# Kernel tuning notes

Measured on AMD Instinct MI355X. Metric: run time of the kernel, lower is better.

## Reference

```python
import jax, jax.numpy as jnp
import numpy as np

KNN_K = 16
EPS = 1e-5


def _knn_idx(p, k):
    # p: [B,3,N] -> idx [B,N,k] of nearest neighbors (self excluded)
    pt = jnp.swapaxes(p, 1, 2)                      # [B,N,3]
    xx = jnp.sum(pt * pt, axis=-1)                  # [B,N]
    inner = jnp.einsum('bnd,bmd->bnm', pt, pt)      # [B,N,N]
    dist = -(xx[:, :, None] - 2.0 * inner + xx[:, None, :])  # -||pi-pj||^2
    N = pt.shape[1]
    dist = dist - 1e9 * jnp.eye(N, dtype=dist.dtype)
    return jax.lax.top_k(dist, k)[1]


def _ln(x, g, b):
    mu = jnp.mean(x, axis=-1, keepdims=True)
    var = jnp.mean((x - mu) ** 2, axis=-1, keepdims=True)
    return (x - mu) * jax.lax.rsqrt(var + EPS) * g + b


_gather = jax.vmap(lambda a, i: a[i])  # a:[N,C], i:[N,k] -> [N,k,C]


def setup_inputs() -> dict:
    key = jax.random.key(0)
    ks = jax.random.split(key, 24)
    Cin, C, B, N = 64, 128, 8, 2048
    s = lambda k_, shp, fan: jax.random.normal(k_, shp, jnp.float32) * (1.0 / np.sqrt(fan))
    return {
        'x': jax.random.normal(ks[0], (B, Cin, N), jnp.float32),
        'p': jax.random.normal(ks[1], (B, 3, N), jnp.float32),
        'Win': s(ks[2], (C, Cin), Cin), 'bin_': jnp.zeros((C,), jnp.float32),
        'Wq': s(ks[3], (C, C), C), 'Wk': s(ks[4], (C, C), C), 'Wv': s(ks[5], (C, C), C),
        'Wd1': s(ks[6], (C, 3), 3), 'bd1': jnp.zeros((C,), jnp.float32),
        'Wd2': s(ks[7], (C, C), C), 'bd2': jnp.zeros((C,), jnp.float32),
        'Wa': s(ks[8], (C, C), C), 'ba': jnp.zeros((C,), jnp.float32),
        'g1': jnp.ones((C,), jnp.float32), 'b1': jnp.zeros((C,), jnp.float32),
        'g2': jnp.ones((C,), jnp.float32), 'b2': jnp.zeros((C,), jnp.float32),
        'Wf1': s(ks[9], (4 * C, C), C), 'bf1': jnp.zeros((4 * C,), jnp.float32),
        'Wf2': s(ks[10], (C, 4 * C), 4 * C), 'bf2': jnp.zeros((C,), jnp.float32),
    }


def reference(x, p, Win, bin_, Wq, Wk, Wv, Wd1, bd1, Wd2, bd2, Wa, ba,
              g1, b1, g2, b2, Wf1, bf1, Wf2, bf2) -> jnp.ndarray:
    B, _, N = x.shape
    k = min(KNN_K, max(1, N - 1))
    # in_proj (conv1x1 == per-point linear); work in [B,N,C]
    h = jnp.einsum('oc,bcn->bno', Win, x) + bin_          # [B,N,C]
    hn = _ln(h, g1, b1)
    idx = _knn_idx(p, k)                                  # [B,N,k] (int)
    q = hn @ Wq.T                                         # [B,N,C]
    k_all = hn @ Wk.T
    v_all = hn @ Wv.T
    k_j = _gather(k_all, idx)                             # [B,N,k,C]
    v_j = _gather(v_all, idx)
    pt = jnp.swapaxes(p, 1, 2)                            # [B,N,3]
    p_j = _gather(pt, idx)                                # [B,N,k,3]
    rel = pt[:, :, None, :] - p_j                         # [B,N,k,3]
    d = jax.nn.relu(rel @ Wd1.T + bd1) @ Wd2.T + bd2      # [B,N,k,C]
    logits = (q[:, :, None, :] - k_j + d) @ Wa.T + ba     # [B,N,k,C]
    a = jax.nn.softmax(logits, axis=2)                    # softmax over neighbors
    y = jnp.sum(a * (v_j + d), axis=2)                    # [B,N,C]
    h = h + y
    h2 = _ln(h, g2, b2)
    h = h + jax.nn.relu(h2 @ Wf1.T + bf1) @ Wf2.T + bf2
    return jnp.swapaxes(h, 1, 2)                          # [B,C,N]
```

## Files before the change

### kernel.cpp

```cpp
#include <hip/hip_runtime.h>

typedef __bf16 bf16_t;
typedef __bf16 bf16x8 __attribute__((ext_vector_type(8)));
typedef __bf16 bf16x2 __attribute__((ext_vector_type(2)));
typedef float  f32x4  __attribute__((ext_vector_type(4)));

#define MFMA16(a,b,c) __builtin_amdgcn_mfma_f32_16x16x32_bf16((a),(b),(c),0,0,0)

#define BB 8
#define NN 2048
#define CC 128
#define CIN 64
#define KNB 16
#define BNT (BB*NN)

static __device__ __forceinline__ int remap256(int x) { return ((x & 7) << 5) | (x >> 3); }

static __device__ __forceinline__ bf16x8 cvt8(const float* src) {
  f32x4 a0 = *(const f32x4*)src;
  f32x4 a1 = *(const f32x4*)(src + 4);
  bf16x8 fr;
  fr[0] = (__bf16)a0[0]; fr[1] = (__bf16)a0[1]; fr[2] = (__bf16)a0[2]; fr[3] = (__bf16)a0[3];
  fr[4] = (__bf16)a1[0]; fr[5] = (__bf16)a1[1]; fr[6] = (__bf16)a1[2]; fr[7] = (__bf16)a1[3];
  return fr;
}

__global__ __launch_bounds__(256) void inproj_ln_k(
    const float* __restrict__ x, const float* __restrict__ Win, const float* __restrict__ bin,
    const float* __restrict__ g1, const float* __restrict__ b1,
    float* __restrict__ h, bf16_t* __restrict__ hnb) {
  __shared__ bf16_t As[64 * 72];
  __shared__ bf16_t Bs[128 * 72];
  __shared__ float hs[64 * 132];
  int t = threadIdx.x;
  int lane = t & 63, w = t >> 6, quad = lane >> 4, l15 = lane & 15;
  int mBase = remap256(blockIdx.x) * 64;
  int b = mBase >> 11, n0 = mBase & (NN - 1);
  const float* xb = x + (size_t)b * CIN * NN;
  {
    int k = t >> 2, part = t & 3;
    #pragma unroll
    for (int i = 0; i < 4; ++i) {
      f32x4 v = *(const f32x4*)(xb + (size_t)k * NN + n0 + part * 16 + i * 4);
      #pragma unroll
      for (int j2 = 0; j2 < 4; ++j2) As[(part * 16 + i * 4 + j2) * 72 + k] = (__bf16)v[j2];
    }
  }
  {
    int row = t >> 1, seg = (t & 1) * 32;
    #pragma unroll
    for (int i = 0; i < 4; ++i)
      *(bf16x8*)(&Bs[row * 72 + seg + i * 8]) = cvt8(Win + (size_t)row * CIN + seg + i * 8);
  }
  __syncthreads();
  f32x4 acc[2][4] = {};
  #pragma unroll
  for (int s = 0; s < 2; ++s) {
    bf16x8 af[4];
    #pragma unroll
    for (int mt = 0; mt < 4; ++mt)
      af[mt] = *(const bf16x8*)(&As[(mt * 16 + l15) * 72 + s * 32 + quad * 8]);
    #pragma unroll
    for (int t2 = 0; t2 < 2; ++t2) {
      bf16x8 bfr = *(const bf16x8*)(&Bs[((w * 2 + t2) * 16 + l15) * 72 + s * 32 + quad * 8]);
      #pragma unroll
      for (int mt = 0; mt < 4; ++mt) acc[t2][mt] = MFMA16(af[mt], bfr, acc[t2][mt]);
    }
  }
  #pragma unroll
  for (int t2 = 0; t2 < 2; ++t2) {
    int col = (w * 2 + t2) * 16 + l15;
    float bv = bin[col];
    #pragma unroll
    for (int mt = 0; mt < 4; ++mt)
      #pragma unroll
      for (int reg = 0; reg < 4; ++reg)
        hs[(mt * 16 + quad * 4 + reg) * 132 + col] = acc[t2][mt][reg] + bv;
  }
  __syncthreads();
  {
    int row = t >> 2, c0 = (t & 3) * 32;
    float v[32];
    #pragma unroll
    for (int i = 0; i < 8; ++i) *(f32x4*)(v + i * 4) = *(const f32x4*)(&hs[row * 132 + c0 + i * 4]);
    float s1 = 0.f, s2 = 0.f;
    #pragma unroll
    for (int i = 0; i < 32; ++i) { s1 += v[i]; s2 += v[i] * v[i]; }
    s1 += __shfl_xor(s1, 1); s1 += __shfl_xor(s1, 2);
    s2 += __shfl_xor(s2, 1); s2 += __shfl_xor(s2, 2);
    float mu = s1 * (1.f / CC);
    float var = s2 * (1.f / CC) - mu * mu;
    float rs = rsqrtf(var + 1e-5f);
    float* hrow = h + (size_t)(mBase + row) * CC + c0;
    #pragma unroll
    for (int i = 0; i < 8; ++i) *(f32x4*)(hrow + i * 4) = *(const f32x4*)(v + i * 4);
    bf16_t* hnrow = hnb + (size_t)(mBase + row) * CC + c0;
    #pragma unroll
    for (int i = 0; i < 4; ++i) {
      f32x4 g4a = ((const f32x4*)g1)[(c0 >> 2) + i * 2],     g4b = ((const f32x4*)g1)[(c0 >> 2) + i * 2 + 1];
      f32x4 b4a = ((const f32x4*)b1)[(c0 >> 2) + i * 2],     b4b = ((const f32x4*)b1)[(c0 >> 2) + i * 2 + 1];
      bf16x8 o;
      #pragma unroll
      for (int j = 0; j < 4; ++j) o[j]     = (__bf16)((v[i * 8 + j]     - mu) * rs * g4a[j] + b4a[j]);
      #pragma unroll
      for (int j = 0; j < 4; ++j) o[4 + j] = (__bf16)((v[i * 8 + 4 + j] - mu) * rs * g4b[j] + b4b[j]);
      *(bf16x8*)(hnrow + i * 8) = o;
    }
  }
}

static __device__ __forceinline__ void cas(double& a, double& b) {
  double lo = fmin(a, b), hi = fmax(a, b); a = lo; b = hi;
}
#define S8(K,o) \
  cas(K[o+0],K[o+1]); cas(K[o+2],K[o+3]); cas(K[o+4],K[o+5]); cas(K[o+6],K[o+7]); \
  cas(K[o+0],K[o+2]); cas(K[o+1],K[o+3]); cas(K[o+4],K[o+6]); cas(K[o+5],K[o+7]); \
  cas(K[o+1],K[o+2]); cas(K[o+5],K[o+6]); \
  cas(K[o+0],K[o+4]); cas(K[o+1],K[o+5]); cas(K[o+2],K[o+6]); cas(K[o+3],K[o+7]); \
  cas(K[o+2],K[o+4]); cas(K[o+3],K[o+5]); \
  cas(K[o+1],K[o+2]); cas(K[o+3],K[o+4]); cas(K[o+5],K[o+6]);
#define M8(K,a,b) \
  K[a+0]=fmin(K[a+0],K[b+7]); K[a+1]=fmin(K[a+1],K[b+6]); K[a+2]=fmin(K[a+2],K[b+5]); K[a+3]=fmin(K[a+3],K[b+4]); \
  K[a+4]=fmin(K[a+4],K[b+3]); K[a+5]=fmin(K[a+5],K[b+2]); K[a+6]=fmin(K[a+6],K[b+1]); K[a+7]=fmin(K[a+7],K[b+0]); \
  cas(K[a+0],K[a+4]); cas(K[a+1],K[a+5]); cas(K[a+2],K[a+6]); cas(K[a+3],K[a+7]); \
  cas(K[a+0],K[a+2]); cas(K[a+1],K[a+3]); cas(K[a+4],K[a+6]); cas(K[a+5],K[a+7]); \
  cas(K[a+0],K[a+1]); cas(K[a+2],K[a+3]); cas(K[a+4],K[a+5]); cas(K[a+6],K[a+7]);

static __device__ void knn_impl(float* sp, const float* __restrict__ p,
                                int* __restrict__ idxo, int bid) {
  float* px = sp; float* py = sp + NN; float* pz = sp + 2 * NN;
  int t = threadIdx.x;
  int b = bid >> 9;
  int g = bid & 511;
  const float* pb = p + (size_t)b * 3 * NN;
  for (int i = t; i < NN; i += 256) { px[i] = pb[i]; py[i] = pb[NN + i]; pz[i] = pb[2 * NN + i]; }
  __syncthreads();
  int w = t >> 6, lane = t & 63;
  int n = g * 4 + w;
  float pnx = px[n], pny = py[n], pnz = pz[n];
  double key[32];
  #pragma unroll
  for (int s = 0; s < 32; ++s) {
    int m = s * 64 + lane;
    float dx = pnx - px[m], dy = pny - py[m], dz = pnz - pz[m];
    float dist = dx * dx + dy * dy + dz * dz;
    unsigned db = (m == n) ? 0x7F800000u : __float_as_uint(dist);
    key[s] = __hiloint2double((int)db, m);
  }
  S8(key, 0); S8(key, 8); S8(key, 16); S8(key, 24);
  M8(key, 0, 8); M8(key, 16, 24); M8(key, 0, 16);
  const double DINF = __hiloint2double(0x7F900000, 0);
  int* myout = idxo + ((size_t)b * NN + n) * KNB;
  #pragma unroll 1
  for (int r = 0; r < 16; ++r) {
    double gm = key[0];
    #pragma unroll
    for (int off = 1; off < 64; off <<= 1) {
      double o = __shfl_xor(gm, off);
      gm = fmin(gm, o);
    }
    if (lane == 0) myout[r] = __double2loint(gm);
    bool win = (key[0] == gm);
    key[0] = win ? key[1] : key[0];
    key[1] = win ? key[2] : key[1];
    key[2] = win ? key[3] : key[2];
    key[3] = win ? key[4] : key[3];
    key[4] = win ? key[5] : key[4];
    key[5] = win ? key[6] : key[5];
    key[6] = win ? key[7] : key[6];
    key[7] = win ? DINF   : key[7];
  }
}

template<int EPI>
static __device__ void gemm_body2(bf16_t* As, bf16_t* Bs,
    const bf16_t* __restrict__ Ab, const float* __restrict__ W, const float* __restrict__ bias,
    float* __restrict__ outF, bf16_t* __restrict__ outB, const float* __restrict__ resid,
    int mBase, int nBase, int Ncol, int Kdim) {
  int t = threadIdx.x;
  int lane = t & 63, w = t >> 6, quad = lane >> 4, l15 = lane & 15;
  int r = t >> 2, segbase = (t & 3) * 32;
  f32x4 acc[4] = {{0,0,0,0},{0,0,0,0},{0,0,0,0},{0,0,0,0}};
  for (int k0 = 0; k0 < Kdim; k0 += 128) {
    __syncthreads();
    #pragma unroll
    for (int i = 0; i < 4; ++i) {
      int seg = segbase + i * 8;
      *(bf16x8*)(&As[r * 136 + seg]) = *(const bf16x8*)(Ab + (size_t)(mBase + r) * Kdim + k0 + seg);
      *(bf16x8*)(&Bs[r * 136 + seg]) = cvt8(W + (size_t)(nBase + r) * Kdim + k0 + seg);
    }
    __syncthreads();
    #pragma unroll
    for (int s = 0; s < 4; ++s) {
      bf16x8 bfr = *(const bf16x8*)(&Bs[(w * 16 + l15) * 136 + s * 32 + quad * 8]);
      #pragma unroll
      for (int mt = 0; mt < 4; ++mt) {
        bf16x8 afr = *(const bf16x8*)(&As[(mt * 16 + l15) * 136 + s * 32 + quad * 8]);
        acc[mt] = MFMA16(afr, bfr, acc[mt]);
      }
    }
  }
  int n = nBase + w * 16 + l15;
  float bv = bias ? bias[n] : 0.f;
  #pragma unroll
  for (int mt = 0; mt < 4; ++mt) {
    #pragma unroll
    for (int reg = 0; reg < 4; ++reg) {
      int m = mBase + mt * 16 + quad * 4 + reg;
      float val = acc[mt][reg] + bv;
      if (EPI == 0) {
        outF[(size_t)m * Ncol + n] = val;
      } else if (EPI == 1) {
        outB[(size_t)m * Ncol + n] = (__bf16)fmaxf(val, 0.f);
      } else if (EPI == 3) {
        outB[(size_t)m * Ncol + n] = (__bf16)val;
      } else {
        val += resid[(size_t)m * CC + n];
        int bo = m >> 11, np = m & (NN - 1);
        outF[((size_t)bo * CC + n) * NN + np] = val;
      }
    }
  }
}

template<int EPI>
__global__ __launch_bounds__(256) void gemm_k(
    const bf16_t* __restrict__ Ab, const float* __restrict__ W, const float* __restrict__ bias,
    float* __restrict__ outF, bf16_t* __restrict__ outB, const float* __restrict__ resid,
    int Ncol, int Kdim) {
  __shared__ bf16_t As[64 * 136];
  __shared__ bf16_t Bs[64 * 136];
  gemm_body2<EPI>(As, Bs, Ab, W, bias, outF, outB, resid,
                  remap256(blockIdx.x) * 64, blockIdx.y * 64, Ncol, Kdim);
}

__global__ __launch_bounds__(256) void knn_qkv_k(
    const float* __restrict__ p, int* __restrict__ idxo,
    const bf16_t* __restrict__ hnb,
    const float* __restrict__ Wq, const float* __restrict__ Wk, const float* __restrict__ Wv,
    float* __restrict__ q, bf16_t* __restrict__ kb, bf16_t* __restrict__ vb) {
  __shared__ __align__(16) char smem[2 * 64 * 136 * 2];
  if (blockIdx.x < 4096) {
    knn_impl((float*)smem, p, idxo, blockIdx.x);
  } else {
    bf16_t* As = (bf16_t*)smem;
    bf16_t* Bs = As + 64 * 136;
    int bx = blockIdx.x - 4096;
    int yy = bx >> 8, xx = bx & 255;
    int sel = yy >> 1;
    int mB = remap256(xx) * 64, nB = (yy & 1) * 64;
    if (sel == 0)      gemm_body2<0>(As, Bs, hnb, Wq, nullptr, q,  nullptr, nullptr, mB, nB, CC, CC);
    else if (sel == 1) gemm_body2<3>(As, Bs, hnb, Wk, nullptr, nullptr, kb, nullptr, mB, nB, CC, CC);
    else               gemm_body2<3>(As, Bs, hnb, Wv, nullptr, nullptr, vb, nullptr, mB, nB, CC, CC);
  }
}

__global__ __launch_bounds__(256, 3) void attn_k(
    const float* __restrict__ qbuf, const bf16_t* __restrict__ kbuf, const bf16_t* __restrict__ vbuf,
    const float* __restrict__ p, const int* __restrict__ idx,
    const float* __restrict__ Wd1, const float* __restrict__ bd1,
    const float* __restrict__ Wd2, const float* __restrict__ bd2,
    const float* __restrict__ Wa, const float* __restrict__ ba,
    const float* __restrict__ g2, const float* __restrict__ b2,
    const float* __restrict__ h, float* __restrict__ hres, bf16_t* __restrict__ h2) {
  __shared__ bf16_t ts[64 * 136];
  __shared__ float hrs[4 * 128];
  __shared__ f32x4 wd1s[128];
  __shared__ f32x4 rels4[64];
  __shared__ int idxs[64];
  int t = threadIdx.x;
  int lane = t & 63, w = t >> 6, quad = lane >> 4, l15 = lane & 15;
  int batch = blockIdx.x & 7, grp = blockIdx.x >> 3;
  int bn0 = batch * NN + grp * 4;
  int b = batch;
  const float* pb = p + (size_t)b * 3 * NN;
  int col0 = w * 32 + l15;
  int col1 = col0 + 16;

  bf16x8 Bd[2][4];
  #pragma unroll
  for (int t2 = 0; t2 < 2; ++t2) {
    int row = w * 32 + t2 * 16 + l15;
    #pragma unroll
    for (int s = 0; s < 4; ++s)
      Bd[t2][s] = cvt8(Wd2 + (size_t)row * CC + s * 32 + quad * 8);
  }

  if (t < 64) {
    int jj = idx[(size_t)bn0 * KNB + t];
    idxs[t] = jj;
    int npt = grp * 4 + (t >> 4);
    f32x4 rv;
    rv[0] = pb[npt]          - pb[jj];
    rv[1] = pb[NN + npt]     - pb[NN + jj];
    rv[2] = pb[2 * NN + npt] - pb[2 * NN + jj];
    rv[3] = 0.f;
    rels4[t] = rv;
  }
  if (t < 128) {
    f32x4 wv;
    wv[0] = Wd1[t * 3]; wv[1] = Wd1[t * 3 + 1]; wv[2] = Wd1[t * 3 + 2]; wv[3] = bd1[t];
    wd1s[t] = wv;
  }
  __syncthreads();

  float qv[2][4];
  #pragma unroll
  for (int mt = 0; mt < 4; ++mt) {
    qv[0][mt] = qbuf[(size_t)(bn0 + mt) * CC + col0];
    qv[1][mt] = qbuf[(size_t)(bn0 + mt) * CC + col1];
  }
  float kreg[2][4][4];
  #pragma unroll
  for (int mt = 0; mt < 4; ++mt)
    #pragma unroll
    for (int reg = 0; reg < 4; ++reg) {
      size_t base = (size_t)(b * NN + idxs[mt * 16 + quad * 4 + reg]) * CC;
      kreg[0][mt][reg] = (float)kbuf[base + col0];
      kreg[1][mt][reg] = (float)kbuf[base + col1];
    }

  f32x4 relv[4];
  #pragma unroll
  for (int mt = 0; mt < 4; ++mt) relv[mt] = rels4[mt * 16 + l15];
  f32x4 accd[2][4] = {};
  #pragma unroll
  for (int s = 0; s < 4; ++s) {
    bf16x8 af[4];
    #pragma unroll
    for (int j = 0; j < 8; ++j) {
      f32x4 wv = wd1s[s * 32 + quad * 8 + j];
      #pragma unroll
      for (int mt = 0; mt < 4; ++mt) {
        float tv = fmaf(wv[0], relv[mt][0], fmaf(wv[1], relv[mt][1], fmaf(wv[2], relv[mt][2], wv[3])));
        af[mt][j] = (__bf16)fmaxf(tv, 0.f);
      }
    }
    #pragma unroll
    for (int t2 = 0; t2 < 2; ++t2)
      #pragma unroll
      for (int mt = 0; mt < 4; ++mt)
        accd[t2][mt] = MFMA16(af[mt], Bd[t2][s], accd[t2][mt]);
  }

  {
    float b2v0 = bd2[col0], b2v1 = bd2[col1];
    #pragma unroll
    for (int mt = 0; mt < 4; ++mt)
      #pragma unroll
      for (int reg = 0; reg < 4; ++reg) {
        int row = mt * 16 + quad * 4 + reg;
        float d0 = accd[0][mt][reg] + b2v0;
        float d1 = accd[1][mt][reg] + b2v1;
        accd[0][mt][reg] = d0;
        accd[1][mt][reg] = d1;
        ts[row * 136 + col0] = (__bf16)(qv[0][mt] - kreg[0][mt][reg] + d0);
        ts[row * 136 + col1] = (__bf16)(qv[1][mt] - kreg[1][mt][reg] + d1);
      }
  }
  __syncthreads();

  float vreg[2][4][4];
  #pragma unroll
  for (int mt = 0; mt < 4; ++mt)
    #pragma unroll
    for (int reg = 0; reg < 4; ++reg) {
      size_t base = (size_t)(b * NN + idxs[mt * 16 + quad * 4 + reg]) * CC;
      vreg[0][mt][reg] = (float)vbuf[base + col0];
      vreg[1][mt][reg] = (float)vbuf[base + col1];
    }
  float hv[2][4];
  if (quad == 0) {
    #pragma unroll
    for (int mt = 0; mt < 4; ++mt) {
      hv[0][mt] = h[(size_t)(bn0 + mt) * CC + col0];
      hv[1][mt] = h[(size_t)(bn0 + mt) * CC + col1];
    }
  }
  bf16x8 Ba[2][4];
  #pragma unroll
  for (int t2 = 0; t2 < 2; ++t2) {
    int row = w * 32 + t2 * 16 + l15;
    #pragma unroll
    for (int s = 0; s < 4; ++s)
      Ba[t2][s] = cvt8(Wa + (size_t)row * CC + s * 32 + quad * 8);
  }

  f32x4 accl[2][4] = {};
  #pragma unroll
  for (int s = 0; s < 4; ++s) {
    bf16x8 af[4];
    #pragma unroll
    for (int mt = 0; mt < 4; ++mt)
      af[mt] = *(const bf16x8*)(&ts[(mt * 16 + l15) * 136 + s * 32 + quad * 8]);
    #pragma unroll
    for (int t2 = 0; t2 < 2; ++t2)
      #pragma unroll
      for (int mt = 0; mt < 4; ++mt)
        accl[t2][mt] = MFMA16(af[mt], Ba[t2][s], accl[t2][mt]);
  }

  #pragma unroll
  for (int t2 = 0; t2 < 2; ++t2) {
    int col = t2 ? col1 : col0;
    float bav = ba[col];
    #pragma unroll
    for (int mt = 0; mt < 4; ++mt) {
      float lv0 = accl[t2][mt][0] + bav, lv1 = accl[t2][mt][1] + bav;
      float lv2 = accl[t2][mt][2] + bav, lv3 = accl[t2][mt][3] + bav;
      float mx = fmaxf(fmaxf(lv0, lv1), fmaxf(lv2, lv3));
      mx = fmaxf(mx, __shfl_xor(mx, 16));
      mx = fmaxf(mx, __shfl_xor(mx, 32));
      float e0 = __expf(lv0 - mx), e1 = __expf(lv1 - mx);
      float e2 = __expf(lv2 - mx), e3 = __expf(lv3 - mx);
      float ss = e0 + e1 + e2 + e3;
      ss += __shfl_xor(ss, 16); ss += __shfl_xor(ss, 32);
      float yv = e0 * (vreg[t2][mt][0] + accd[t2][mt][0])
               + e1 * (vreg[t2][mt][1] + accd[t2][mt][1])
               + e2 * (vreg[t2][mt][2] + accd[t2][mt][2])
               + e3 * (vreg[t2][mt][3] + accd[t2][mt][3]);
      yv += __shfl_xor(yv, 16); yv += __shfl_xor(yv, 32);
      if (quad == 0) {
        float hvv = hv[t2][mt] + yv / ss;
        hres[(size_t)(bn0 + mt) * CC + col] = hvv;
        hrs[mt * 128 + col] = hvv;
      }
    }
  }
  __syncthreads();

  {
    int c0 = lane * 2;
    float v0 = hrs[w * 128 + c0], v1 = hrs[w * 128 + c0 + 1];
    float s1 = v0 + v1, s2 = v0 * v0 + v1 * v1;
    #pragma unroll
    for (int off = 1; off < 64; off <<= 1) { s1 += __shfl_xor(s1, off); s2 += __shfl_xor(s2, off); }
    float mu = s1 * (1.f / CC);
    float var = s2 * (1.f / CC) - mu * mu;
    float rs = rsqrtf(var + 1e-5f);
    bf16x2 o;
    o[0] = (__bf16)((v0 - mu) * rs * g2[c0] + b2[c0]);
    o[1] = (__bf16)((v1 - mu) * rs * g2[c0 + 1] + b2[c0 + 1]);
    *(bf16x2*)(h2 + (size_t)(bn0 + w) * CC + c0) = o;
  }
}

extern "C" void kernel_launch(void* const* d_in, const int* in_sizes, int n_in,
                              void* d_out, int out_size, void* d_ws, size_t ws_size,
                              hipStream_t stream) {
  const float* x   = (const float*)d_in[0];
  const float* p   = (const float*)d_in[1];
  const float* Win = (const float*)d_in[2];
  const float* bin = (const float*)d_in[3];
  const float* Wq  = (const float*)d_in[4];
  const float* Wk  = (const float*)d_in[5];
  const float* Wv  = (const float*)d_in[6];
  const float* Wd1 = (const float*)d_in[7];
  const float* bd1 = (const float*)d_in[8];
  const float* Wd2 = (const float*)d_in[9];
  const float* bd2 = (const float*)d_in[10];
  const float* Wa  = (const float*)d_in[11];
  const float* ba  = (const float*)d_in[12];
  const float* g1  = (const float*)d_in[13];
  const float* b1  = (const float*)d_in[14];
  const float* g2  = (const float*)d_in[15];
  const float* b2  = (const float*)d_in[16];
  const float* Wf1 = (const float*)d_in[17];
  const float* bf1 = (const float*)d_in[18];
  const float* Wf2 = (const float*)d_in[19];
  const float* bf2 = (const float*)d_in[20];
  float* out = (float*)d_out;

  const size_t SZ = (size_t)BNT * CC;
  float* wsf = (float*)d_ws;
  float*  h    = wsf;
  bf16_t* hnb  = (bf16_t*)(wsf + SZ);
  float*  hres = wsf + SZ;
  float*  q    = wsf + 2 * SZ;
  bf16_t* kb   = (bf16_t*)(wsf + 3 * SZ);
  bf16_t* vb   = kb + SZ;
  bf16_t* g    = (bf16_t*)(wsf + 2 * SZ);
  bf16_t* h2   = (bf16_t*)(wsf + 4 * SZ);
  int*    idxw = (int*)(wsf + 4 * SZ + SZ / 2);

  inproj_ln_k<<<BNT / 64, 256, 0, stream>>>(x, Win, bin, g1, b1, h, hnb);
  knn_qkv_k<<<4096 + 1536, 256, 0, stream>>>(p, idxw, hnb, Wq, Wk, Wv, q, kb, vb);
  attn_k<<<BNT / 4, 256, 0, stream>>>(q, kb, vb, p, idxw, Wd1, bd1, Wd2, bd2, Wa, ba,
                                      g2, b2, h, hres, h2);
  gemm_k<1><<<dim3(BNT / 64, 8), 256, 0, stream>>>(h2, Wf1, bf1, nullptr, g, nullptr, 4 * CC, CC);
  gemm_k<2><<<dim3(BNT / 64, 2), 256, 0, stream>>>(g, Wf2, bf2, out, nullptr, hres, CC, 4 * CC);
}
```

Measured before the change: 295.1 us.

## Pre-convert weights to bf16 once and shrink GEMM K-tile to 32

Adds a small kernel that converts the fp32 weight matrices (Wq, Wk, Wv, Wd2, Wa, Wf1, Wf2) to bf16 in workspace at the start of each call. GEMMs and the attention kernel then load bf16 weights directly instead of converting per block, which cuts redundant conversion work and global weight traffic. The GEMM body also drops from a 128-wide K tile to a 32-wide one, which shrinks LDS use and may raise occupancy, but it adds more barriers per K step and gives less MFMA work between syncs. The knn_qkv shared buffer is resized to the knn requirement. The extra launch adds a little overhead.

```diff
diff --git a/kernel.cpp b/kernel.cpp
--- a/kernel.cpp
+++ b/kernel.cpp
@@ -23,6 +23,23 @@
   fr[0] = (__bf16)a0[0]; fr[1] = (__bf16)a0[1]; fr[2] = (__bf16)a0[2]; fr[3] = (__bf16)a0[3];
   fr[4] = (__bf16)a1[0]; fr[5] = (__bf16)a1[1]; fr[6] = (__bf16)a1[2]; fr[7] = (__bf16)a1[3];
   return fr;
+}
+
+__global__ __launch_bounds__(256) void compw_k(
+    const float* __restrict__ Wq, const float* __restrict__ Wk, const float* __restrict__ Wv,
+    const float* __restrict__ Wd2, const float* __restrict__ Wa,
+    const float* __restrict__ Wf1, const float* __restrict__ Wf2,
+    bf16_t* __restrict__ Wqb, bf16_t* __restrict__ Wkb, bf16_t* __restrict__ Wvb,
+    bf16_t* __restrict__ Wd2b, bf16_t* __restrict__ Wab,
+    bf16_t* __restrict__ Wf1b, bf16_t* __restrict__ Wf2b) {
+  int mat = blockIdx.y;
+  int nel = (mat >= 5) ? 65536 : 16384;
+  const float* S = mat == 0 ? Wq : mat == 1 ? Wk : mat == 2 ? Wv : mat == 3 ? Wd2
+                 : mat == 4 ? Wa : mat == 5 ? Wf1 : Wf2;
+  bf16_t* D = mat == 0 ? Wqb : mat == 1 ? Wkb : mat == 2 ? Wvb : mat == 3 ? Wd2b
+            : mat == 4 ? Wab : mat == 5 ? Wf1b : Wf2b;
+  for (int i = blockIdx.x * 256 + threadIdx.x; i * 8 < nel; i += 2048)
+    *(bf16x8*)(D + i * 8) = cvt8(S + i * 8);
 }
 
 __global__ __launch_bounds__(256) void inproj_ln_k(
@@ -173,31 +190,24 @@
 }
 
 template<int EPI>
-static __device__ void gemm_body2(bf16_t* As, bf16_t* Bs,
-    const bf16_t* __restrict__ Ab, const float* __restrict__ W, const float* __restrict__ bias,
+static __device__ void gemm_body(bf16_t* As, bf16_t* Bs,
+    const bf16_t* __restrict__ Ab, const bf16_t* __restrict__ Wb, const float* __restrict__ bias,
     float* __restrict__ outF, bf16_t* __restrict__ outB, const float* __restrict__ resid,
     int mBase, int nBase, int Ncol, int Kdim) {
   int t = threadIdx.x;
   int lane = t & 63, w = t >> 6, quad = lane >> 4, l15 = lane & 15;
-  int r = t >> 2, segbase = (t & 3) * 32;
+  int r = t >> 2, seg = (t & 3) * 8;
   f32x4 acc[4] = {{0,0,0,0},{0,0,0,0},{0,0,0,0},{0,0,0,0}};
-  for (int k0 = 0; k0 < Kdim; k0 += 128) {
+  for (int k0 = 0; k0 < Kdim; k0 += 32) {
     __syncthreads();
-    #pragma unroll
-    for (int i = 0; i < 4; ++i) {
-      int seg = segbase + i * 8;
-      *(bf16x8*)(&As[r * 136 + seg]) = *(const bf16x8*)(Ab + (size_t)(mBase + r) * Kdim + k0 + seg);
-      *(bf16x8*)(&Bs[r * 136 + seg]) = cvt8(W + (size_t)(nBase + r) * Kdim + k0 + seg);
-    }
+    *(bf16x8*)(&As[r * 40 + seg]) = *(const bf16x8*)(Ab + (size_t)(mBase + r) * Kdim + k0 + seg);
+    *(bf16x8*)(&Bs[r * 40 + seg]) = *(const bf16x8*)(Wb + (size_t)(nBase + r) * Kdim + k0 + seg);
     __syncthreads();
-    #pragma unroll
-    for (int s = 0; s < 4; ++s) {
-      bf16x8 bfr = *(const bf16x8*)(&Bs[(w * 16 + l15) * 136 + s * 32 + quad * 8]);
-      #pragma unroll
-      for (int mt = 0; mt < 4; ++mt) {
-        bf16x8 afr = *(const bf16x8*)(&As[(mt * 16 + l15) * 136 + s * 32 + quad * 8]);
-        acc[mt] = MFMA16(afr, bfr, acc[mt]);
-      }
+    bf16x8 bfr = *(const bf16x8*)(&Bs[(w * 16 + l15) * 40 + quad * 8]);
+    #pragma unroll
+    for (int mt = 0; mt < 4; ++mt) {
+      bf16x8 afr = *(const bf16x8*)(&As[(mt * 16 + l15) * 40 + quad * 8]);
+      acc[mt] = MFMA16(afr, bfr, acc[mt]);
     }
   }
   int n = nBase + w * 16 + l15;
@@ -225,33 +235,33 @@
 
 template<int EPI>
 __global__ __launch_bounds__(256) void gemm_k(
-    const bf16_t* __restrict__ Ab, const float* __restrict__ W, const float* __restrict__ bias,
+    const bf16_t* __restrict__ Ab, const bf16_t* __restrict__ Wb, const float* __restrict__ bias,
     float* __restrict__ outF, bf16_t* __restrict__ outB, const float* __restrict__ resid,
     int Ncol, int Kdim) {
-  __shared__ bf16_t As[64 * 136];
-  __shared__ bf16_t Bs[64 * 136];
-  gemm_body2<EPI>(As, Bs, Ab, W, bias, outF, outB, resid,
-                  remap256(blockIdx.x) * 64, blockIdx.y * 64, Ncol, Kdim);
+  __shared__ bf16_t As[64 * 40];
+  __shared__ bf16_t Bs[64 * 40];
+  gemm_body<EPI>(As, Bs, Ab, Wb, bias, outF, outB, resid,
+                 remap256(blockIdx.x) * 64, blockIdx.y * 64, Ncol, Kdim);
 }
 
 __global__ __launch_bounds__(256) void knn_qkv_k(
     const float* __restrict__ p, int* __restrict__ idxo,
     const bf16_t* __restrict__ hnb,
-    const float* __restrict__ Wq, const float* __restrict__ Wk, const float* __restrict__ Wv,
+    const bf16_t* __restrict__ Wqb, const bf16_t* __restrict__ Wkb, const bf16_t* __restrict__ Wvb,
     float* __restrict__ q, bf16_t* __restrict__ kb, bf16_t* __restrict__ vb) {
-  __shared__ __align__(16) char smem[2 * 64 * 136 * 2];
+  __shared__ __align__(16) char smem[3 * NN * 4];
   if (blockIdx.x < 4096) {
     knn_impl((float*)smem, p, idxo, blockIdx.x);
   } else {
     bf16_t* As = (bf16_t*)smem;
-    bf16_t* Bs = As + 64 * 136;
+    bf16_t* Bs = As + 64 * 40;
     int bx = blockIdx.x - 4096;
     int yy = bx >> 8, xx = bx & 255;
     int sel = yy >> 1;
     int mB = remap256(xx) * 64, nB = (yy & 1) * 64;
-    if (sel == 0)      gemm_body2<0>(As, Bs, hnb, Wq, nullptr, q,  nullptr, nullptr, mB, nB, CC, CC);
-    else if (sel == 1) gemm_body2<3>(As, Bs, hnb, Wk, nullptr, nullptr, kb, nullptr, mB, nB, CC, CC);
-    else               gemm_body2<3>(As, Bs, hnb, Wv, nullptr, nullptr, vb, nullptr, mB, nB, CC, CC);
+    if (sel == 0)      gemm_body<0>(As, Bs, hnb, Wqb, nullptr, q,  nullptr, nullptr, mB, nB, CC, CC);
+    else if (sel == 1) gemm_body<3>(As, Bs, hnb, Wkb, nullptr, nullptr, kb, nullptr, mB, nB, CC, CC);
+    else               gemm_body<3>(As, Bs, hnb, Wvb, nullptr, nullptr, vb, nullptr, mB, nB, CC, CC);
   }
 }
 
@@ -259,8 +269,8 @@
     const float* __restrict__ qbuf, const bf16_t* __restrict__ kbuf, const bf16_t* __restrict__ vbuf,
     const float* __restrict__ p, const int* __restrict__ idx,
     const float* __restrict__ Wd1, const float* __restrict__ bd1,
-    const float* __restrict__ Wd2, const float* __restrict__ bd2,
-    const float* __restrict__ Wa, const float* __restrict__ ba,
+    const bf16_t* __restrict__ Wd2b, const float* __restrict__ bd2,
+    const bf16_t* __restrict__ Wab, const float* __restrict__ ba,
     const float* __restrict__ g2, const float* __restrict__ b2,
     const float* __restrict__ h, float* __restrict__ hres, bf16_t* __restrict__ h2) {
   __shared__ bf16_t ts[64 * 136];
@@ -283,7 +293,7 @@
     int row = w * 32 + t2 * 16 + l15;
     #pragma unroll
     for (int s = 0; s < 4; ++s)
-      Bd[t2][s] = cvt8(Wd2 + (size_t)row * CC + s * 32 + quad * 8);
+      Bd[t2][s] = *(const bf16x8*)(Wd2b + (size_t)row * CC + s * 32 + quad * 8);
   }
 
   if (t < 64) {
@@ -383,7 +393,7 @@
     int row = w * 32 + t2 * 16 + l15;
     #pragma unroll
     for (int s = 0; s < 4; ++s)
-      Ba[t2][s] = cvt8(Wa + (size_t)row * CC + s * 32 + quad * 8);
+      Ba[t2][s] = *(const bf16x8*)(Wab + (size_t)row * CC + s * 32 + quad * 8);
   }
 
   f32x4 accl[2][4] = {};
@@ -482,11 +492,20 @@
   bf16_t* g    = (bf16_t*)(wsf + 2 * SZ);
   bf16_t* h2   = (bf16_t*)(wsf + 4 * SZ);
   int*    idxw = (int*)(wsf + 4 * SZ + SZ / 2);
-
+  bf16_t* Wqb  = (bf16_t*)(idxw + (size_t)BNT * KNB);
+  bf16_t* Wkb  = Wqb  + 16384;
+  bf16_t* Wvb  = Wkb  + 16384;
+  bf16_t* Wd2b = Wvb  + 16384;
+  bf16_t* Wab  = Wd2b + 16384;
+  bf16_t* Wf1b = Wab  + 16384;
+  bf16_t* Wf2b = Wf1b + 65536;
+
+  compw_k<<<dim3(8, 7), 256, 0, stream>>>(Wq, Wk, Wv, Wd2, Wa, Wf1, Wf2,
+                                          Wqb, Wkb, Wvb, Wd2b, Wab, Wf1b, Wf2b);
   inproj_ln_k<<<BNT / 64, 256, 0, stream>>>(x, Win, bin, g1, b1, h, hnb);
-  knn_qkv_k<<<4096 + 1536, 256, 0, stream>>>(p, idxw, hnb, Wq, Wk, Wv, q, kb, vb);
-  attn_k<<<BNT / 4, 256, 0, stream>>>(q, kb, vb, p, idxw, Wd1, bd1, Wd2, bd2, Wa, ba,
+  knn_qkv_k<<<4096 + 1536, 256, 0, stream>>>(p, idxw, hnb, Wqb, Wkb, Wvb, q, kb, vb);
+  attn_k<<<BNT / 4, 256, 0, stream>>>(q, kb, vb, p, idxw, Wd1, bd1, Wd2b, bd2, Wab, ba,
                                       g2, b2, h, hres, h2);
-  gemm_k<1><<<dim3(BNT / 64, 8), 256, 0, stream>>>(h2, Wf1, bf1, nullptr, g, nullptr, 4 * CC, CC);
-  gemm_k<2><<<dim3(BNT / 64, 2), 256, 0, stream>>>(g, Wf2, bf2, out, nullptr, hres, CC, 4 * CC);
-}
+  gemm_k<1><<<dim3(BNT / 64, 8), 256, 0, stream>>>(h2, Wf1b, bf1, nullptr, g, nullptr, 4 * CC, CC);
+  gemm_k<2><<<dim3(BNT / 64, 2), 256, 0, stream>>>(g, Wf2b, bf2, out, nullptr, hres, CC, 4 * CC);
+}
```

Result: faster. 266.0 us (-9.9%).
